# Performance work log

Hardware: AMD Instinct MI355X
Metric: run time of the kernel (lower is better)

Reference implementation:

```python
import jax, jax.numpy as jnp
import numpy as np

GRID = (8192, 8192)   # 2D lattice, *dims
NDIM = 2              # links.shape[0]
P_LINK = 0.45         # subcritical bond probability -> finite clusters, bounded step count


def setup_inputs() -> dict:
    key = jax.random.key(0)
    k1, k2 = jax.random.split(key)
    # links[i] marks an open bond between site x and its +1 neighbour along axis i
    links = jax.random.uniform(k1, (NDIM,) + GRID) < P_LINK
    seed_idx = jax.random.randint(k2, (NDIM,), 0, GRID[0]).astype(jnp.int32)
    return {"links": links, "seed_idx": seed_idx}


def _flood_fill(links, seed_idx):
    """Faithful port of ClusterSelection.from_seed_idx: BFS-style roll+mask
    expansion iterated to fixed point via lax.while_loop."""
    ndim = links.shape[0]
    grid = links.shape[1:]
    selected0 = jnp.zeros(grid, dtype=bool).at[tuple(seed_idx)].set(True)

    def cond(carry):
        _, is_done, _ = carry
        return ~is_done

    def body(carry):
        sel0, _, steps = carry
        sel = sel0
        for i in range(ndim):  # unrolled over the (small, static) ndim
            # sites whose -1-neighbour or self is selected can use bond i
            links_to_try = sel0 | jnp.roll(sel0, -1, i)
            links_sel = links_to_try & links[i]
            # a taken bond marks both of its endpoints
            links_sel = links_sel | jnp.roll(links_sel, 1, i)
            sel = sel | links_sel
        is_done = (sel ^ sel0).sum() == 0
        return sel, is_done, steps + 1

    sel, _, steps = jax.lax.while_loop(
        cond, body, (selected0, jnp.array(False), jnp.array(0, jnp.int32))
    )
    return sel, steps


def reference(links, seed_idx):
    sel, _steps = _flood_fill(links, seed_idx)
    return sel
```

## Files before the change

### kernel.cpp

```cpp
#include <hip/hip_runtime.h>
#include <stdint.h>

#define GW 8192
#define GMASK 8191
#define PLANE 67108864ULL
#define TPD 128
#define TMASK 127
#define NTILES 16384
#define QCAP 16384
#define QMASK 16383
#define WPR 128

#define WS_BITMAP 4096
#define WS_TFEVER (WS_BITMAP + 8388608)

#define OUT_U4 16777216u

typedef unsigned long long u64;
typedef unsigned int u32;
typedef unsigned int u32x4 __attribute__((ext_vector_type(4)));

__global__ void clear_bitmap_kernel(uint4* __restrict__ p, int n) {
    int i = blockIdx.x * blockDim.x + threadIdx.x;
    if (i < n) p[i] = make_uint4(0, 0, 0, 0);
}

__device__ __forceinline__ u32 nib4(u32 w) {
    return (((w & 0x01010101u) * 0x01020408u) >> 24) & 0xFu;
}
__device__ __forceinline__ u64 pack_row_b8(const unsigned char* p) {
    const uint4* q = (const uint4*)p;
    u64 w = 0;
#pragma unroll
    for (int i = 0; i < 4; i++) {
        uint4 v = q[i];
        u64 nb = (u64)(nib4(v.x) | (nib4(v.y) << 4) | (nib4(v.z) << 8) | (nib4(v.w) << 12));
        w |= nb << (16 * i);
    }
    return w;
}
__device__ __forceinline__ u64 pack_row_b32(const u32* p) {
    u64 w = 0;
#pragma unroll
    for (int k = 0; k < 16; k++) {
        uint4 v = ((const uint4*)p)[k];
        u64 nb = (u64)((v.x != 0) | ((v.y != 0) << 1) | ((v.z != 0) << 2) | ((v.w != 0) << 3));
        w |= nb << (4 * k);
    }
    return w;
}

__global__ void __launch_bounds__(1024)
mega_kernel(const unsigned char* __restrict__ links8,
            const int* __restrict__ seed_idx,
            unsigned char* __restrict__ ws,
            u32x4* __restrict__ outv) {
    volatile __shared__ unsigned short q[QCAP];
    __shared__ u32 tflags[NTILES / 32];
    __shared__ u32 tfever[NTILES / 32];
    __shared__ int s_qhead, s_qtail, s_active, s_mode, s_c1, s_c3;

    if (blockIdx.x != 0) {
        u32 gtid = (blockIdx.x - 1) * 1024 + threadIdx.x;
        u32 stride = (gridDim.x - 1) * 1024;
        u32x4 z = (u32x4)(0u);
        for (u32 i = gtid; i < OUT_U4; i += stride)
            __builtin_nontemporal_store(z, &outv[i]);
        return;
    }

    u64* bitmap = (u64*)(ws + WS_BITMAP);
    const int tid = threadIdx.x;
    const int ln  = tid & 63;

    for (int i = tid; i < QCAP; i += 1024) q[i] = 0xFFFF;
    for (int i = tid; i < NTILES / 32; i += 1024) { tflags[i] = 0; tfever[i] = 0; }
    if (tid == 0) { s_c1 = 0; s_c3 = 0; s_qhead = 0; s_qtail = 0; s_active = 0; }
    __syncthreads();

    int l1c = 0, l3c = 0;
    for (int i = tid; i < 16384; i += 1024) {
        if (links8[i]) { int m = i & 3; if (m == 1) l1c++; else if (m == 3) l3c++; }
    }
    atomicAdd(&s_c1, l1c);
    atomicAdd(&s_c3, l3c);
    __syncthreads();
    if (tid == 0) {
        s_mode = (s_c1 > 0) ? 0 : ((s_c3 > 0) ? 2 : 1);
        int sr = seed_idx[0] & GMASK, sc = seed_idx[1] & GMASK;
        atomicOr(&bitmap[(u64)sr * WPR + (sc >> 6)], 1ull << (sc & 63));
        int t = (sr >> 6) * TPD + (sc >> 6);
        tflags[t >> 5] = 1u << (t & 31);
        tfever[t >> 5] = 1u << (t & 31);
        q[0] = (unsigned short)t;
        s_qtail = 1; s_active = 1;
    }
    __syncthreads();

    const int mode = s_mode;
    const unsigned char* p0b = links8;
    const unsigned char* p1b = links8 + PLANE;
    const u32* p0w = (const u32*)links8;
    const u32* p1w = (const u32*)(links8 + PLANE * 4);

    auto enq = [&](int t2) {
        u32 bit = 1u << (t2 & 31);
        atomicOr(&tfever[t2 >> 5], bit);
        u32 old = atomicOr(&tflags[t2 >> 5], bit);
        if (!(old & bit)) {
            atomicAdd(&s_active, 1);
            int pos = atomicAdd(&s_qtail, 1) & QMASK;
            q[pos] = (unsigned short)t2;
        }
    };

    long long guard = 0;
    while (true) {
        int t = -1;
        if (ln == 0) {
            while (true) {
                if (atomicAdd(&s_active, 0) == 0) break;
                int h  = atomicAdd(&s_qhead, 0);
                int tl = atomicAdd(&s_qtail, 0);
                if (h != tl && atomicCAS(&s_qhead, h, h + 1) == h) {
                    int pos = h & QMASK;
                    unsigned short v;
                    long long g2 = 0;
                    while ((v = q[pos]) == 0xFFFF) { if (++g2 > 400000000LL) break; }
                    q[pos] = 0xFFFF;
                    t = v;
                    break;
                }
                if (++guard > 400000000LL) break;
            }
        }
        t = __shfl(t, 0);
        if (t < 0) break;

        const int tR = t >> 7, tC = t & TMASK;
        const int c0 = tC * 64;
        if (ln == 0) atomicAnd(&tflags[t >> 5], ~(1u << (t & 31)));
        __threadfence_block();

        const int gr = tR * 64 + ln;
        u64* wp = &bitmap[(u64)gr * WPR + tC];
        u64 loaded = *(volatile u64*)wp;

        u64 l0, l1;
        if (mode == 0) {
            l0 = pack_row_b8(p0b + (u64)gr * GW + tC * 64);
            l1 = pack_row_b8(p1b + (u64)gr * GW + tC * 64);
        } else {
            l0 = pack_row_b32(p0w + (u64)gr * GW + tC * 64);
            l1 = pack_row_b32(p1w + (u64)gr * GW + tC * 64);
        }

        u64 P0 = l1 & 0x7FFFFFFFFFFFFFFFull;
        u64 P1 = P0 & (P0 >> 1);
        u64 P2 = P1 & (P1 >> 2);
        u64 P3 = P2 & (P2 >> 4);
        u64 P4 = P3 & (P3 >> 8);
        u64 P5 = P4 & (P4 >> 16);
        u64 D0 = (ln < 63) ? l0 : 0ull;
        u64 D1 = D0 & __shfl_down(D0, 1);
        u64 D2 = D1 & __shfl_down(D1, 2);
        u64 D3 = D2 & __shfl_down(D2, 4);
        u64 D4 = D3 & __shfl_down(D3, 8);
        u64 D5 = D4 & __shfl_down(D4, 16);

        u64 sel = loaded;
        while (true) {
            u64 old = sel;
            sel |= (sel & P0) << 1;  sel |= (sel >> 1)  & P0;
            sel |= (sel & P1) << 2;  sel |= (sel >> 2)  & P1;
            sel |= (sel & P2) << 4;  sel |= (sel >> 4)  & P2;
            sel |= (sel & P3) << 8;  sel |= (sel >> 8)  & P3;
            sel |= (sel & P4) << 16; sel |= (sel >> 16) & P4;
            sel |= (sel & P5) << 32; sel |= (sel >> 32) & P5;
            sel |= __shfl_up(sel & D0, 1);  sel |= __shfl_down(sel, 1)  & D0;
            sel |= __shfl_up(sel & D1, 2);  sel |= __shfl_down(sel, 2)  & D1;
            sel |= __shfl_up(sel & D2, 4);  sel |= __shfl_down(sel, 4)  & D2;
            sel |= __shfl_up(sel & D3, 8);  sel |= __shfl_down(sel, 8)  & D3;
            sel |= __shfl_up(sel & D4, 16); sel |= __shfl_down(sel, 16) & D4;
            sel |= __shfl_up(sel & D5, 32); sel |= __shfl_down(sel, 32) & D5;
            if (__ballot(sel != old) == 0ull) break;
        }

        u64 newbits = sel & ~loaded;
        if (newbits) atomicOr(wp, newbits);

        bool rnew = false, lnew = false;
        if ((sel >> 63) & (l1 >> 63) & 1ull) {
            u64 old = atomicOr(&bitmap[(u64)gr * WPR + ((tC + 1) & TMASK)], 1ull);
            rnew = !(old & 1ull);
        }
        if (sel & 1ull) {
            u64 lcol2 = (u64)((c0 - 1) & GMASK);
            bool lopen = (mode == 0) ? (p1b[(u64)gr * GW + lcol2] != 0)
                                     : (p1w[(u64)gr * GW + lcol2] != 0);
            if (lopen) {
                u64 old = atomicOr(&bitmap[(u64)gr * WPR + ((tC - 1) & TMASK)], 1ull << 63);
                lnew = !(old & (1ull << 63));
            }
        }
        u64 rmask = __ballot(rnew), lmask = __ballot(lnew);

        const int ga = (tR * 64 - 1) & GMASK;
        u64 top_sel = __shfl(sel, 0);
        u64 umask = 0;
        if (top_sel) {
            bool bopen = ((top_sel >> ln) & 1) &&
                ((mode == 0) ? (p0b[(u64)ga * GW + c0 + ln] != 0)
                             : (p0w[(u64)ga * GW + c0 + ln] != 0));
            umask = __ballot(bopen);
        }
        u64 unew = 0;
        if (ln == 0 && umask) {
            u64 old = atomicOr(&bitmap[(u64)ga * WPR + tC], umask);
            unew = umask & ~old;
        }
        u64 dmask = sel & l0;
        const int gb = (tR * 64 + 64) & GMASK;
        u64 dnew = 0;
        if (ln == 63 && dmask) {
            u64 old = atomicOr(&bitmap[(u64)gb * WPR + tC], dmask);
            dnew = dmask & ~old;
        }

        if (ln == 0  && rmask) enq(tR * TPD + ((tC + 1) & TMASK));
        if (ln == 1  && lmask) enq(tR * TPD + ((tC - 1) & TMASK));
        if (ln == 0  && unew)  enq(((tR - 1) & TMASK) * TPD + tC);
        if (ln == 63 && dnew)  enq(((tR + 1) & TMASK) * TPD + tC);

        if (ln == 0) atomicSub(&s_active, 1);
    }

    __syncthreads();
    for (int i = tid; i < NTILES / 32; i += 1024)
        ((u32*)(ws + WS_TFEVER))[i] = tfever[i];
}

__global__ void __launch_bounds__(256)
writeout_sparse(const unsigned char* __restrict__ ws, u32x4* __restrict__ ob) {
    const u64* bitmap = (const u64*)(ws + WS_BITMAP);
    const u32* tf = (const u32*)(ws + WS_TFEVER);
    for (int t = blockIdx.x; t < NTILES; t += gridDim.x) {
        if (!((tf[t >> 5] >> (t & 31)) & 1u)) continue;
        int tR = t >> 7, tC = t & TMASK;
        for (int i = threadIdx.x; i < 1024; i += 256) {
            int row = i >> 4, c4 = i & 15;
            u64 w = bitmap[(u64)(tR * 64 + row) * WPR + tC];
            u32 nb = (u32)(w >> (c4 * 4)) & 0xFu;
            u32x4 v;
            v.x = nb & 1; v.y = (nb >> 1) & 1; v.z = (nb >> 2) & 1; v.w = (nb >> 3) & 1;
            __builtin_nontemporal_store(
                v, &ob[(u64)(tR * 64 + row) * 2048 + tC * 16 + c4]);
        }
    }
}

extern "C" void kernel_launch(void* const* d_in, const int* in_sizes, int n_in,
                              void* d_out, int out_size, void* d_ws, size_t ws_size,
                              hipStream_t stream) {
    const unsigned char* links = (const unsigned char*)d_in[0];
    const int* seed = (const int*)d_in[1];
    unsigned char* ws = (unsigned char*)d_ws;

    u64* bitmap = (u64*)(ws + WS_BITMAP);

    clear_bitmap_kernel<<<2048, 256, 0, stream>>>((uint4*)bitmap, 524288);
    mega_kernel<<<256, 1024, 0, stream>>>(links, seed, ws, (u32x4*)d_out);
    writeout_sparse<<<1024, 256, 0, stream>>>(ws, (u32x4*)d_out);
}
```

Baseline: 657.9 us.

## Process one newly activated neighbour tile directly instead of enqueueing it

After finishing a tile, the wave now continues straight onto one newly activated neighbour tile, chosen in priority right, left, down, up. The other activated neighbours are still enqueued, and the continued tile's ever-touched flag is set directly. This is meant to cut shared-queue enqueue/dequeue traffic and atomic contention on the work queue. The intra-tile closure loop also splits left and right (and up and down) propagation into independent chains to shorten dependency depth. The trade-off is that work becomes less evenly spread across waves and the control flow is more complex.

```diff
diff --git a/kernel.cpp b/kernel.cpp
--- a/kernel.cpp
+++ b/kernel.cpp
@@ -137,100 +137,125 @@
         t = __shfl(t, 0);
         if (t < 0) break;
 
-        const int tR = t >> 7, tC = t & TMASK;
-        const int c0 = tC * 64;
-        if (ln == 0) atomicAnd(&tflags[t >> 5], ~(1u << (t & 31)));
-        __threadfence_block();
-
-        const int gr = tR * 64 + ln;
-        u64* wp = &bitmap[(u64)gr * WPR + tC];
-        u64 loaded = *(volatile u64*)wp;
-
-        u64 l0, l1;
-        if (mode == 0) {
-            l0 = pack_row_b8(p0b + (u64)gr * GW + tC * 64);
-            l1 = pack_row_b8(p1b + (u64)gr * GW + tC * 64);
-        } else {
-            l0 = pack_row_b32(p0w + (u64)gr * GW + tC * 64);
-            l1 = pack_row_b32(p1w + (u64)gr * GW + tC * 64);
-        }
-
-        u64 P0 = l1 & 0x7FFFFFFFFFFFFFFFull;
-        u64 P1 = P0 & (P0 >> 1);
-        u64 P2 = P1 & (P1 >> 2);
-        u64 P3 = P2 & (P2 >> 4);
-        u64 P4 = P3 & (P3 >> 8);
-        u64 P5 = P4 & (P4 >> 16);
-        u64 D0 = (ln < 63) ? l0 : 0ull;
-        u64 D1 = D0 & __shfl_down(D0, 1);
-        u64 D2 = D1 & __shfl_down(D1, 2);
-        u64 D3 = D2 & __shfl_down(D2, 4);
-        u64 D4 = D3 & __shfl_down(D3, 8);
-        u64 D5 = D4 & __shfl_down(D4, 16);
-
-        u64 sel = loaded;
+        bool popped = true;
         while (true) {
-            u64 old = sel;
-            sel |= (sel & P0) << 1;  sel |= (sel >> 1)  & P0;
-            sel |= (sel & P1) << 2;  sel |= (sel >> 2)  & P1;
-            sel |= (sel & P2) << 4;  sel |= (sel >> 4)  & P2;
-            sel |= (sel & P3) << 8;  sel |= (sel >> 8)  & P3;
-            sel |= (sel & P4) << 16; sel |= (sel >> 16) & P4;
-            sel |= (sel & P5) << 32; sel |= (sel >> 32) & P5;
-            sel |= __shfl_up(sel & D0, 1);  sel |= __shfl_down(sel, 1)  & D0;
-            sel |= __shfl_up(sel & D1, 2);  sel |= __shfl_down(sel, 2)  & D1;
-            sel |= __shfl_up(sel & D2, 4);  sel |= __shfl_down(sel, 4)  & D2;
-            sel |= __shfl_up(sel & D3, 8);  sel |= __shfl_down(sel, 8)  & D3;
-            sel |= __shfl_up(sel & D4, 16); sel |= __shfl_down(sel, 16) & D4;
-            sel |= __shfl_up(sel & D5, 32); sel |= __shfl_down(sel, 32) & D5;
-            if (__ballot(sel != old) == 0ull) break;
-        }
-
-        u64 newbits = sel & ~loaded;
-        if (newbits) atomicOr(wp, newbits);
-
-        bool rnew = false, lnew = false;
-        if ((sel >> 63) & (l1 >> 63) & 1ull) {
-            u64 old = atomicOr(&bitmap[(u64)gr * WPR + ((tC + 1) & TMASK)], 1ull);
-            rnew = !(old & 1ull);
-        }
-        if (sel & 1ull) {
-            u64 lcol2 = (u64)((c0 - 1) & GMASK);
-            bool lopen = (mode == 0) ? (p1b[(u64)gr * GW + lcol2] != 0)
-                                     : (p1w[(u64)gr * GW + lcol2] != 0);
-            if (lopen) {
-                u64 old = atomicOr(&bitmap[(u64)gr * WPR + ((tC - 1) & TMASK)], 1ull << 63);
-                lnew = !(old & (1ull << 63));
-            }
-        }
-        u64 rmask = __ballot(rnew), lmask = __ballot(lnew);
-
-        const int ga = (tR * 64 - 1) & GMASK;
-        u64 top_sel = __shfl(sel, 0);
-        u64 umask = 0;
-        if (top_sel) {
-            bool bopen = ((top_sel >> ln) & 1) &&
-                ((mode == 0) ? (p0b[(u64)ga * GW + c0 + ln] != 0)
-                             : (p0w[(u64)ga * GW + c0 + ln] != 0));
-            umask = __ballot(bopen);
-        }
-        u64 unew = 0;
-        if (ln == 0 && umask) {
-            u64 old = atomicOr(&bitmap[(u64)ga * WPR + tC], umask);
-            unew = umask & ~old;
-        }
-        u64 dmask = sel & l0;
-        const int gb = (tR * 64 + 64) & GMASK;
-        u64 dnew = 0;
-        if (ln == 63 && dmask) {
-            u64 old = atomicOr(&bitmap[(u64)gb * WPR + tC], dmask);
-            dnew = dmask & ~old;
-        }
-
-        if (ln == 0  && rmask) enq(tR * TPD + ((tC + 1) & TMASK));
-        if (ln == 1  && lmask) enq(tR * TPD + ((tC - 1) & TMASK));
-        if (ln == 0  && unew)  enq(((tR - 1) & TMASK) * TPD + tC);
-        if (ln == 63 && dnew)  enq(((tR + 1) & TMASK) * TPD + tC);
+            const int tR = t >> 7, tC = t & TMASK;
+            const int c0 = tC * 64;
+            if (popped && ln == 0) atomicAnd(&tflags[t >> 5], ~(1u << (t & 31)));
+            __threadfence_block();
+
+            const int gr = tR * 64 + ln;
+            u64* wp = &bitmap[(u64)gr * WPR + tC];
+            u64 loaded = *(volatile u64*)wp;
+
+            u64 l0, l1;
+            if (mode == 0) {
+                l0 = pack_row_b8(p0b + (u64)gr * GW + tC * 64);
+                l1 = pack_row_b8(p1b + (u64)gr * GW + tC * 64);
+            } else {
+                l0 = pack_row_b32(p0w + (u64)gr * GW + tC * 64);
+                l1 = pack_row_b32(p1w + (u64)gr * GW + tC * 64);
+            }
+
+            u64 P0 = l1 & 0x7FFFFFFFFFFFFFFFull;
+            u64 P1 = P0 & (P0 >> 1);
+            u64 P2 = P1 & (P1 >> 2);
+            u64 P3 = P2 & (P2 >> 4);
+            u64 P4 = P3 & (P3 >> 8);
+            u64 P5 = P4 & (P4 >> 16);
+            u64 D0 = (ln < 63) ? l0 : 0ull;
+            u64 D1 = D0 & __shfl_down(D0, 1);
+            u64 D2 = D1 & __shfl_down(D1, 2);
+            u64 D3 = D2 & __shfl_down(D2, 4);
+            u64 D4 = D3 & __shfl_down(D3, 8);
+            u64 D5 = D4 & __shfl_down(D4, 16);
+
+            u64 sel = loaded;
+            while (true) {
+                u64 old = sel;
+                u64 a = sel, b = sel;
+                a |= (a & P0) << 1;   b |= (b >> 1)  & P0;
+                a |= (a & P1) << 2;   b |= (b >> 2)  & P1;
+                a |= (a & P2) << 4;   b |= (b >> 4)  & P2;
+                a |= (a & P3) << 8;   b |= (b >> 8)  & P3;
+                a |= (a & P4) << 16;  b |= (b >> 16) & P4;
+                a |= (a & P5) << 32;  b |= (b >> 32) & P5;
+                sel = a | b;
+                u64 d = sel, e = sel;
+                d |= __shfl_up(d & D0, 1);   e |= __shfl_down(e, 1)  & D0;
+                d |= __shfl_up(d & D1, 2);   e |= __shfl_down(e, 2)  & D1;
+                d |= __shfl_up(d & D2, 4);   e |= __shfl_down(e, 4)  & D2;
+                d |= __shfl_up(d & D3, 8);   e |= __shfl_down(e, 8)  & D3;
+                d |= __shfl_up(d & D4, 16);  e |= __shfl_down(e, 16) & D4;
+                d |= __shfl_up(d & D5, 32);  e |= __shfl_down(e, 32) & D5;
+                sel = d | e;
+                if (__ballot(sel != old) == 0ull) break;
+            }
+
+            u64 newbits = sel & ~loaded;
+            if (newbits) atomicOr(wp, newbits);
+
+            bool rnew = false, lnew = false;
+            if ((sel >> 63) & (l1 >> 63) & 1ull) {
+                u64 old = atomicOr(&bitmap[(u64)gr * WPR + ((tC + 1) & TMASK)], 1ull);
+                rnew = !(old & 1ull);
+            }
+            if (sel & 1ull) {
+                u64 lcol2 = (u64)((c0 - 1) & GMASK);
+                bool lopen = (mode == 0) ? (p1b[(u64)gr * GW + lcol2] != 0)
+                                         : (p1w[(u64)gr * GW + lcol2] != 0);
+                if (lopen) {
+                    u64 old = atomicOr(&bitmap[(u64)gr * WPR + ((tC - 1) & TMASK)],
+                                       1ull << 63);
+                    lnew = !(old & (1ull << 63));
+                }
+            }
+            u64 rmask = __ballot(rnew), lmask = __ballot(lnew);
+
+            const int ga = (tR * 64 - 1) & GMASK;
+            u64 top_sel = __shfl(sel, 0);
+            u64 umask = 0;
+            if (top_sel) {
+                bool bopen = ((top_sel >> ln) & 1) &&
+                    ((mode == 0) ? (p0b[(u64)ga * GW + c0 + ln] != 0)
+                                 : (p0w[(u64)ga * GW + c0 + ln] != 0));
+                umask = __ballot(bopen);
+            }
+            u64 unew = 0;
+            if (ln == 0 && umask) {
+                u64 old = atomicOr(&bitmap[(u64)ga * WPR + tC], umask);
+                unew = umask & ~old;
+            }
+            u64 dmask = sel & l0;
+            const int gb = (tR * 64 + 64) & GMASK;
+            u64 dnew = 0;
+            if (ln == 63 && dmask) {
+                u64 old = atomicOr(&bitmap[(u64)gb * WPR + tC], dmask);
+                dnew = dmask & ~old;
+            }
+            u64 uany = __ballot(unew != 0);
+            u64 dany = __ballot(dnew != 0);
+
+            const int tRt = tR * TPD + ((tC + 1) & TMASK);
+            const int tLt = tR * TPD + ((tC - 1) & TMASK);
+            const int tUt = ((tR - 1) & TMASK) * TPD + tC;
+            const int tDt = ((tR + 1) & TMASK) * TPD + tC;
+
+            bool cR = rmask != 0;
+            bool cL = !cR && lmask != 0;
+            bool cD = !cR && !cL && dany != 0;
+            bool cU = !cR && !cL && !cD && uany != 0;
+
+            if (ln == 1 && lmask && !cL) enq(tLt);
+            if (ln == 2 && uany && !cU)  enq(tUt);
+            if (ln == 3 && dany && !cD)  enq(tDt);
+
+            int tn = cR ? tRt : cL ? tLt : cD ? tDt : cU ? tUt : -1;
+            if (tn < 0) break;
+            if (ln == 0) atomicOr(&tfever[tn >> 5], 1u << (tn & 31));
+            t = tn;
+            popped = false;
+        }
 
         if (ln == 0) atomicSub(&s_active, 1);
     }
```

Result: no change. 667.7 us (+1.5%).
